# Kernel optimization log

Hardware: AMD Instinct MI355X
Metric: run time of the kernel (lower is better)

The kernel has to match this reference:

```python
import jax, jax.numpy as jnp
import numpy as np
import math

EPS = 1e-5  # BatchNorm eps; eval mode with running_mean=0, running_var=1


def maxpool(x, k, p):
    return jax.lax.reduce_window(x, -jnp.inf, jax.lax.max,
                                 (1, 1, k, k), (1, 1, 1, 1),
                                 ((0, 0), (0, 0), (p, p), (p, p)))


def conv1x1(x, w, b=None):
    # x: [B,Cin,H,W], w: [Cout,Cin]
    y = jnp.einsum('oi,bihw->bohw', w, x)
    if b is not None:
        y = y + b[None, :, None, None]
    return y


def bn_eval(x, g, b):
    scale = g / jnp.sqrt(1.0 + EPS)
    return x * scale[None, :, None, None] + b[None, :, None, None]


def setup_inputs() -> dict:
    B, C, H, W = 2, 64, 80, 80
    c1, c2, c3 = 21, 21, 22
    ch = 32  # C//2
    ks = jax.random.split(jax.random.key(0), 16)
    s = 0.05
    inp = {
        'x': jax.random.normal(ks[0], (B, C, H, W), jnp.float32),
        'q1_w': jax.random.normal(ks[1], (c1, c1), jnp.float32) * s,
        'q1_g': jnp.ones((c1,), jnp.float32),
        'q1_b': jnp.zeros((c1,), jnp.float32),
        'q2_w': jax.random.normal(ks[2], (c2, c2), jnp.float32) * s,
        'q2_g': jnp.ones((c2,), jnp.float32),
        'q2_b': jnp.zeros((c2,), jnp.float32),
        'q3_w': jax.random.normal(ks[3], (c3, c3), jnp.float32) * s,
        'q3_g': jnp.ones((c3,), jnp.float32),
        'q3_b': jnp.zeros((c3,), jnp.float32),
        'k_hf_w': jax.random.normal(ks[4], (ch, C), jnp.float32) * s,
        'k_hf_b': jnp.zeros((ch,), jnp.float32),
        'k_lf_w': jax.random.normal(ks[5], (C - ch, C), jnp.float32) * s,
        'k_lf_b': jnp.zeros((C - ch,), jnp.float32),
        'k_fuse_w': jax.random.normal(ks[6], (C, C), jnp.float32) * s,
        'k_fuse_b': jnp.zeros((C,), jnp.float32),
        'v_bn_g': jnp.ones((C,), jnp.float32),
        'v_bn_b': jnp.zeros((C,), jnp.float32),
        'v_w': jax.random.normal(ks[7], (C, C), jnp.float32) * s,
        'v_b': jnp.zeros((C,), jnp.float32),
        'out_w': jax.random.normal(ks[8], (C, C), jnp.float32) * s,
        'out_b': jnp.zeros((C,), jnp.float32),
    }
    return inp


def reference(x, q1_w, q1_g, q1_b, q2_w, q2_g, q2_b, q3_w, q3_g, q3_b,
              k_hf_w, k_hf_b, k_lf_w, k_lf_b, k_fuse_w, k_fuse_b,
              v_bn_g, v_bn_b, v_w, v_b, out_w, out_b):
    B, C, H, W = x.shape
    N = H * W
    c1 = q1_w.shape[0]
    c2 = q2_w.shape[0]
    # Q: ThreeGroupConvQ (split -> 1x1 conv (no bias) -> BN -> ReLU -> concat)
    x1, x2, x3 = jnp.split(x, [c1, c1 + c2], axis=1)
    y1 = jax.nn.relu(bn_eval(conv1x1(x1, q1_w), q1_g, q1_b))
    y2 = jax.nn.relu(bn_eval(conv1x1(x2, q2_w), q2_g, q2_b))
    y3 = jax.nn.relu(bn_eval(conv1x1(x3, q3_w), q3_g, q3_b))
    Q = jnp.concatenate([y1, y2, y3], axis=1)
    # K: ThermalStructureExtractor
    p3 = maxpool(x, 3, 1)
    p5 = maxpool(x, 5, 2)
    low = (p3 + p5) * 0.5
    high = conv1x1(x - low, k_hf_w, k_hf_b)
    lowp = conv1x1(low, k_lf_w, k_lf_b)
    K = conv1x1(jnp.concatenate([high, lowp], axis=1), k_fuse_w, k_fuse_b)
    # V: BN -> 1x1 conv
    V = conv1x1(bn_eval(x, v_bn_g, v_bn_b), v_w, v_b)
    # attention over N = H*W spatial tokens, channel features
    Qc = Q.reshape(B, C, N)
    Kc = K.reshape(B, C, N)
    Vc = V.reshape(B, C, N)
    attn = jax.nn.softmax(
        jnp.einsum('bcn,bcm->bnm', Qc, Kc) / math.sqrt(C), axis=-1)  # [B,N,N]
    out = jnp.einsum('bnm,bcm->bcn', attn, Vc).reshape(B, C, H, W)
    return conv1x1(out, out_w, out_b) + x
```

## Files before the change

kernel.cpp:

```cpp
#include <hip/hip_runtime.h>
#include <hip/hip_bf16.h>


#define BATCH 2
#define CH 64
#define HH 80
#define WW 80
#define NN 6400
#define NT 100
#define KS 5
#define KTPS (NT/KS)
#define EPSV 1e-5f
#define NEGBIG (-1e30f)
#define LOG2E8 0.18033688f

typedef __hip_bfloat16 bf16;
typedef __attribute__((ext_vector_type(8))) short short8;
typedef __attribute__((ext_vector_type(4))) float f4;
#define MFMA16 __builtin_amdgcn_mfma_f32_16x16x32_bf16

__device__ __forceinline__ float b2f(bf16 v){ return __bfloat162float(v); }
__device__ __forceinline__ bf16 f2b(float v){ return __float2bfloat16(v); }
__device__ __forceinline__ ushort f2bu(float v){ return ((__hip_bfloat16_raw)__float2bfloat16(v)).x; }
__device__ __forceinline__ float bu2f(ushort u){
  union { unsigned int i; float f; } w; w.i = ((unsigned int)u) << 16; return w.f;
}
__device__ __forceinline__ unsigned pkbf(float a, float b){
  union { __hip_bfloat162 h2; unsigned u; } cv;
  cv.h2 = __float22bfloat162_rn(make_float2(a, b));
  return cv.u;
}
__device__ __forceinline__ float fexp2(float x){
#if __has_builtin(__builtin_amdgcn_exp2f)
  return __builtin_amdgcn_exp2f(x);
#else
  return exp2f(x);
#endif
}
__device__ __forceinline__ int swz(int row, int colb){
  return row*128 + (colb ^ ((row & 7) << 4));
}

#define OFF_BIAS 0
#define OFF_WH_B 768
#define OFF_LOW_B (768 + 32768)
#define OFF_Q_B   (OFF_LOW_B + BATCH*CH*NN*2)
#define OFF_K_B   (OFF_Q_B   + BATCH*CH*NN*2)
#define OFF_V_B   (OFF_K_B   + BATCH*CH*NN*2)
#define OFF_P_B   (OFF_V_B   + BATCH*CH*NN*2)
#define OFF_ML_B  (OFF_P_B   + BATCH*NT*KS*4096*2)

__global__ __launch_bounds__(256) void setup_fold(
    const float* __restrict__ q1w, const float* __restrict__ q1g, const float* __restrict__ q1b,
    const float* __restrict__ q2w, const float* __restrict__ q2g, const float* __restrict__ q2b,
    const float* __restrict__ q3w, const float* __restrict__ q3g, const float* __restrict__ q3b,
    const float* __restrict__ khw, const float* __restrict__ khb,
    const float* __restrict__ klw, const float* __restrict__ klb,
    const float* __restrict__ kfw, const float* __restrict__ kfb,
    const float* __restrict__ vg,  const float* __restrict__ vbnb,
    const float* __restrict__ vw,  const float* __restrict__ vb,
    const float* __restrict__ outw,
    float* __restrict__ biasf, bf16* __restrict__ wh)
{
  __shared__ __align__(16) float skf[4096];
  __shared__ __align__(16) float skh[2048];
  __shared__ __align__(16) float skl[2048];
  __shared__ __align__(16) float sow[4096];
  __shared__ __align__(16) float svw[4096];
  __shared__ float sbv[64];

  int tid = threadIdx.x;
  int blk = blockIdx.x;
  #pragma unroll
  for (int i = 0; i < 4; ++i) {
    *(float4*)&skf[(i*256 + tid)*4] = *(const float4*)&kfw[(i*256 + tid)*4];
    *(float4*)&sow[(i*256 + tid)*4] = *(const float4*)&outw[(i*256 + tid)*4];
    *(float4*)&svw[(i*256 + tid)*4] = *(const float4*)&vw[(i*256 + tid)*4];
  }
  #pragma unroll
  for (int i = 0; i < 2; ++i) {
    *(float4*)&skh[(i*256 + tid)*4] = *(const float4*)&khw[(i*256 + tid)*4];
    *(float4*)&skl[(i*256 + tid)*4] = *(const float4*)&klw[(i*256 + tid)*4];
  }
  __syncthreads();

  float rs = rsqrtf(1.0f + EPSV);
  if (tid < 64) {
    int j = tid;
    float bvo = vb[j];
    for (int ci2 = 0; ci2 < 64; ++ci2) bvo += svw[j*64 + ci2] * vbnb[ci2];
    sbv[j] = bvo;
  }

  bf16* wq   = wh;
  bf16* wvp  = wh + 4096;
  bf16* wa1  = wh + 8192;
  bf16* wa2m = wh + 12288;

  int t = blk*256 + tid;
  int ci = t & 63, co = t >> 6;
  int o = co*64 + ci;

  float w = 0.f, g;
  if (co < 21)      { g = q1g[co];    w = (ci < 21)              ? q1w[co*21 + ci]            : 0.f; }
  else if (co < 42) { g = q2g[co-21]; w = (ci >= 21 && ci < 42)  ? q2w[(co-21)*21 + (ci-21)]  : 0.f; }
  else              { g = q3g[co-42]; w = (ci >= 42)             ? q3w[(co-42)*22 + (ci-42)]  : 0.f; }
  wq[o] = f2b(w * g * rs * LOG2E8);

  float a1 = 0.f, a2 = 0.f;
  #pragma unroll
  for (int j = 0; j < 32; ++j) {
    a1 += skf[co*64 + j]      * skh[j*64 + ci];
    a2 += skf[co*64 + 32 + j] * skl[j*64 + ci];
  }
  wa1[o]  = f2b(a1);
  wa2m[o] = f2b(a2 - a1);

  float av = 0.f;
  #pragma unroll
  for (int j = 0; j < 64; ++j)
    av += sow[co*64 + j] * svw[j*64 + ci];
  wvp[o] = f2b(av * vg[ci] * rs);

  if (blk == 0 && tid < 64) {
    int c2 = tid;
    float bq;
    if (c2 < 21)      bq = q1b[c2];
    else if (c2 < 42) bq = q2b[c2-21];
    else              bq = q3b[c2-42];
    biasf[c2] = bq * LOG2E8;
    float bk = kfb[c2];
    #pragma unroll
    for (int j = 0; j < 32; ++j) {
      bk += skf[c2*64 + j]      * khb[j];
      bk += skf[c2*64 + 32 + j] * klb[j];
    }
    biasf[64 + c2] = bk;
    float bvp = 0.f;
    #pragma unroll
    for (int j = 0; j < 64; ++j) bvp += sow[c2*64 + j] * sbv[j];
    biasf[128 + c2] = bvp;
  }
}

__global__ __launch_bounds__(256) void pool_low(const float* __restrict__ x,
                                                bf16* __restrict__ lowg)
{
  int t4 = (blockIdx.x*256 + threadIdx.x)*4;
  int bc = t4 / NN; int n = t4 % NN;
  int h = n / WW, w0 = n % WW;
  const float* p = x + bc*NN;
  float m5[4], m3[4];
  #pragma unroll
  for (int j=0;j<4;++j){ m5[j]=NEGBIG; m3[j]=NEGBIG; }
  #pragma unroll
  for (int dh = -2; dh <= 2; ++dh) {
    int hh = h + dh; if (hh < 0 || hh >= HH) continue;
    float r[12];
    const float* row = p + hh*WW;
    if (w0 >= 4)      { float4 a = *(const float4*)&row[w0-4]; r[0]=a.x;r[1]=a.y;r[2]=a.z;r[3]=a.w; }
    else              { r[0]=NEGBIG;r[1]=NEGBIG;r[2]=NEGBIG;r[3]=NEGBIG; }
    { float4 a = *(const float4*)&row[w0]; r[4]=a.x;r[5]=a.y;r[6]=a.z;r[7]=a.w; }
    if (w0 + 7 < WW)  { float4 a = *(const float4*)&row[w0+4]; r[8]=a.x;r[9]=a.y;r[10]=a.z;r[11]=a.w; }
    else              { r[8]=NEGBIG;r[9]=NEGBIG;r[10]=NEGBIG;r[11]=NEGBIG; }
    bool in3 = (dh >= -1 && dh <= 1);
    #pragma unroll
    for (int j=0;j<4;++j) {
      float v3 = fmaxf(fmaxf(r[3+j], r[4+j]), r[5+j]);
      float v5 = fmaxf(fmaxf(r[2+j], v3), r[6+j]);
      m5[j] = fmaxf(m5[j], v5);
      if (in3) m3[j] = fmaxf(m3[j], v3);
    }
  }
  ushort4 o;
  o.x = f2bu(0.5f*(m3[0]+m5[0]));
  o.y = f2bu(0.5f*(m3[1]+m5[1]));
  o.z = f2bu(0.5f*(m3[2]+m5[2]));
  o.w = f2bu(0.5f*(m3[3]+m5[3]));
  *(ushort4*)&lowg[t4] = o;
}

__global__ __launch_bounds__(256, 2) void qkv_kernel(
    const float* __restrict__ x, const float* __restrict__ biasf,
    const bf16* __restrict__ wh, const bf16* __restrict__ lowg,
    bf16* __restrict__ qgT, bf16* __restrict__ kgT, bf16* __restrict__ vgc)
{
  __shared__ __align__(16) char xT[8192];
  __shared__ __align__(16) char lT[8192];
  __shared__ float bias[192];

  int tid = threadIdx.x;
  int blk = blockIdx.x;
  int b = blk / NT, tile = blk % NT;
  int n0 = tile*64;
  int wv = tid >> 6, lane = tid & 63, ln = lane & 15, quad = lane >> 4;

  if (tid < 192) bias[tid] = biasf[tid];

  {
    int cq = tid & 15, nq = tid >> 4;
    const float* xp = x + (size_t)(b*CH + cq*4)*NN + n0 + nq*4;
    float4 x0 = *(const float4*)&xp[0*NN];
    float4 x1 = *(const float4*)&xp[(size_t)1*NN];
    float4 x2 = *(const float4*)&xp[(size_t)2*NN];
    float4 x3 = *(const float4*)&xp[(size_t)3*NN];
    const bf16* lp = lowg + (size_t)(b*CH + cq*4)*NN + n0 + nq*4;
    uint2 l0 = *(const uint2*)&lp[0*NN];
    uint2 l1 = *(const uint2*)&lp[(size_t)1*NN];
    uint2 l2 = *(const uint2*)&lp[(size_t)2*NN];
    uint2 l3 = *(const uint2*)&lp[(size_t)3*NN];
    uint2 w;
    w.x = pkbf(x0.x, x1.x); w.y = pkbf(x2.x, x3.x);
    *(uint2*)(xT + swz(nq*4+0, cq*8)) = w;
    w.x = (l0.x & 0xffffu) | ((l1.x & 0xffffu) << 16);
    w.y = (l2.x & 0xffffu) | ((l3.x & 0xffffu) << 16);
    *(uint2*)(lT + swz(nq*4+0, cq*8)) = w;
    w.x = pkbf(x0.y, x1.y); w.y = pkbf(x2.y, x3.y);
    *(uint2*)(xT + swz(nq*4+1, cq*8)) = w;
    w.x = (l0.x >> 16) | ((l1.x >> 16) << 16);
    w.y = (l2.x >> 16) | ((l3.x >> 16) << 16);
    *(uint2*)(lT + swz(nq*4+1, cq*8)) = w;
    w.x = pkbf(x0.z, x1.z); w.y = pkbf(x2.z, x3.z);
    *(uint2*)(xT + swz(nq*4+2, cq*8)) = w;
    w.x = (l0.y & 0xffffu) | ((l1.y & 0xffffu) << 16);
    w.y = (l2.y & 0xffffu) | ((l3.y & 0xffffu) << 16);
    *(uint2*)(lT + swz(nq*4+2, cq*8)) = w;
    w.x = pkbf(x0.w, x1.w); w.y = pkbf(x2.w, x3.w);
    *(uint2*)(xT + swz(nq*4+3, cq*8)) = w;
    w.x = (l0.y >> 16) | ((l1.y >> 16) << 16);
    w.y = (l2.y >> 16) | ((l3.y >> 16) << 16);
    *(uint2*)(lT + swz(nq*4+3, cq*8)) = w;
  }
  __syncthreads();

  short8 xb00 = *(const short8*)(xT + swz(0*16 + ln, quad*16));
  short8 xb01 = *(const short8*)(xT + swz(0*16 + ln, 64 + quad*16));
  short8 xb10 = *(const short8*)(xT + swz(1*16 + ln, quad*16));
  short8 xb11 = *(const short8*)(xT + swz(1*16 + ln, 64 + quad*16));
  short8 xb20 = *(const short8*)(xT + swz(2*16 + ln, quad*16));
  short8 xb21 = *(const short8*)(xT + swz(2*16 + ln, 64 + quad*16));
  short8 xb30 = *(const short8*)(xT + swz(3*16 + ln, quad*16));
  short8 xb31 = *(const short8*)(xT + swz(3*16 + ln, 64 + quad*16));
  short8 xa0 = *(const short8*)(xT + swz(wv*16 + ln, quad*16));
  short8 xa1 = *(const short8*)(xT + swz(wv*16 + ln, 64 + quad*16));

  int cb = wv*16 + quad*4;
  const bf16* wqp  = wh;
  const bf16* wvpp = wh + 4096;
  const bf16* wa1p = wh + 8192;
  const bf16* wa2p = wh + 12288;
  int wrow = (wv*16 + ln)*64;

  {
    {
      short8 w0 = *(const short8*)&wvpp[(0*16 + ln)*64 + quad*8];
      short8 w1 = *(const short8*)&wvpp[(0*16 + ln)*64 + 32 + quad*8];
      float bv = bias[128 + 0*16 + ln];
      f4 a = (f4){bv, bv, bv, bv};
      a = MFMA16(xa0, w0, a, 0, 0, 0);
      a = MFMA16(xa1, w1, a, 0, 0, 0);
      uint2 pk; pk.x = pkbf(a[0], a[1]); pk.y = pkbf(a[2], a[3]);
      *(uint2*)&vgc[(size_t)(b*CH + 0*16 + ln)*NN + n0 + cb] = pk;
    }
    {
      short8 w0 = *(const short8*)&wvpp[(1*16 + ln)*64 + quad*8];
      short8 w1 = *(const short8*)&wvpp[(1*16 + ln)*64 + 32 + quad*8];
      float bv = bias[128 + 1*16 + ln];
      f4 a = (f4){bv, bv, bv, bv};
      a = MFMA16(xa0, w0, a, 0, 0, 0);
      a = MFMA16(xa1, w1, a, 0, 0, 0);
      uint2 pk; pk.x = pkbf(a[0], a[1]); pk.y = pkbf(a[2], a[3]);
      *(uint2*)&vgc[(size_t)(b*CH + 1*16 + ln)*NN + n0 + cb] = pk;
    }
    {
      short8 w0 = *(const short8*)&wvpp[(2*16 + ln)*64 + quad*8];
      short8 w1 = *(const short8*)&wvpp[(2*16 + ln)*64 + 32 + quad*8];
      float bv = bias[128 + 2*16 + ln];
      f4 a = (f4){bv, bv, bv, bv};
      a = MFMA16(xa0, w0, a, 0, 0, 0);
      a = MFMA16(xa1, w1, a, 0, 0, 0);
      uint2 pk; pk.x = pkbf(a[0], a[1]); pk.y = pkbf(a[2], a[3]);
      *(uint2*)&vgc[(size_t)(b*CH + 2*16 + ln)*NN + n0 + cb] = pk;
    }
    {
      short8 w0 = *(const short8*)&wvpp[(3*16 + ln)*64 + quad*8];
      short8 w1 = *(const short8*)&wvpp[(3*16 + ln)*64 + 32 + quad*8];
      float bv = bias[128 + 3*16 + ln];
      f4 a = (f4){bv, bv, bv, bv};
      a = MFMA16(xa0, w0, a, 0, 0, 0);
      a = MFMA16(xa1, w1, a, 0, 0, 0);
      uint2 pk; pk.x = pkbf(a[0], a[1]); pk.y = pkbf(a[2], a[3]);
      *(uint2*)&vgc[(size_t)(b*CH + 3*16 + ln)*NN + n0 + cb] = pk;
    }
  }

  {
    short8 wq0 = *(const short8*)&wqp[wrow + quad*8];
    short8 wq1 = *(const short8*)&wqp[wrow + 32 + quad*8];
    f4 bQ;
    bQ[0] = bias[cb+0]; bQ[1] = bias[cb+1]; bQ[2] = bias[cb+2]; bQ[3] = bias[cb+3];
    {
      f4 a = bQ;
      a = MFMA16(wq0, xb00, a, 0, 0, 0);
      a = MFMA16(wq1, xb01, a, 0, 0, 0);
      uint2 pk;
      pk.x = pkbf(fmaxf(a[0],0.f), fmaxf(a[1],0.f));
      pk.y = pkbf(fmaxf(a[2],0.f), fmaxf(a[3],0.f));
      *(uint2*)&qgT[(size_t)(b*NN + n0 + 0*16 + ln)*64 + cb] = pk;
    }
    {
      f4 a = bQ;
      a = MFMA16(wq0, xb10, a, 0, 0, 0);
      a = MFMA16(wq1, xb11, a, 0, 0, 0);
      uint2 pk;
      pk.x = pkbf(fmaxf(a[0],0.f), fmaxf(a[1],0.f));
      pk.y = pkbf(fmaxf(a[2],0.f), fmaxf(a[3],0.f));
      *(uint2*)&qgT[(size_t)(b*NN + n0 + 1*16 + ln)*64 + cb] = pk;
    }
    {
      f4 a = bQ;
      a = MFMA16(wq0, xb20, a, 0, 0, 0);
      a = MFMA16(wq1, xb21, a, 0, 0, 0);
      uint2 pk;
      pk.x = pkbf(fmaxf(a[0],0.f), fmaxf(a[1],0.f));
      pk.y = pkbf(fmaxf(a[2],0.f), fmaxf(a[3],0.f));
      *(uint2*)&qgT[(size_t)(b*NN + n0 + 2*16 + ln)*64 + cb] = pk;
    }
    {
      f4 a = bQ;
      a = MFMA16(wq0, xb30, a, 0, 0, 0);
      a = MFMA16(wq1, xb31, a, 0, 0, 0);
      uint2 pk;
      pk.x = pkbf(fmaxf(a[0],0.f), fmaxf(a[1],0.f));
      pk.y = pkbf(fmaxf(a[2],0.f), fmaxf(a[3],0.f));
      *(uint2*)&qgT[(size_t)(b*NN + n0 + 3*16 + ln)*64 + cb] = pk;
    }
  }

  {
    short8 wa10 = *(const short8*)&wa1p[wrow + quad*8];
    short8 wa11 = *(const short8*)&wa1p[wrow + 32 + quad*8];
    short8 wm0  = *(const short8*)&wa2p[wrow + quad*8];
    short8 wm1  = *(const short8*)&wa2p[wrow + 32 + quad*8];
    short8 lb00 = *(const short8*)(lT + swz(0*16 + ln, quad*16));
    short8 lb01 = *(const short8*)(lT + swz(0*16 + ln, 64 + quad*16));
    short8 lb10 = *(const short8*)(lT + swz(1*16 + ln, quad*16));
    short8 lb11 = *(const short8*)(lT + swz(1*16 + ln, 64 + quad*16));
    short8 lb20 = *(const short8*)(lT + swz(2*16 + ln, quad*16));
    short8 lb21 = *(const short8*)(lT + swz(2*16 + ln, 64 + quad*16));
    short8 lb30 = *(const short8*)(lT + swz(3*16 + ln, quad*16));
    short8 lb31 = *(const short8*)(lT + swz(3*16 + ln, 64 + quad*16));
    f4 bK;
    bK[0] = bias[64+cb+0]; bK[1] = bias[64+cb+1];
    bK[2] = bias[64+cb+2]; bK[3] = bias[64+cb+3];
    {
      f4 a = bK;
      a = MFMA16(wa10, xb00, a, 0, 0, 0);
      a = MFMA16(wa11, xb01, a, 0, 0, 0);
      a = MFMA16(wm0,  lb00, a, 0, 0, 0);
      a = MFMA16(wm1,  lb01, a, 0, 0, 0);
      uint2 pk; pk.x = pkbf(a[0], a[1]); pk.y = pkbf(a[2], a[3]);
      *(uint2*)&kgT[(size_t)(b*NN + n0 + 0*16 + ln)*64 + cb] = pk;
    }
    {
      f4 a = bK;
      a = MFMA16(wa10, xb10, a, 0, 0, 0);
      a = MFMA16(wa11, xb11, a, 0, 0, 0);
      a = MFMA16(wm0,  lb10, a, 0, 0, 0);
      a = MFMA16(wm1,  lb11, a, 0, 0, 0);
      uint2 pk; pk.x = pkbf(a[0], a[1]); pk.y = pkbf(a[2], a[3]);
      *(uint2*)&kgT[(size_t)(b*NN + n0 + 1*16 + ln)*64 + cb] = pk;
    }
    {
      f4 a = bK;
      a = MFMA16(wa10, xb20, a, 0, 0, 0);
      a = MFMA16(wa11, xb21, a, 0, 0, 0);
      a = MFMA16(wm0,  lb20, a, 0, 0, 0);
      a = MFMA16(wm1,  lb21, a, 0, 0, 0);
      uint2 pk; pk.x = pkbf(a[0], a[1]); pk.y = pkbf(a[2], a[3]);
      *(uint2*)&kgT[(size_t)(b*NN + n0 + 2*16 + ln)*64 + cb] = pk;
    }
    {
      f4 a = bK;
      a = MFMA16(wa10, xb30, a, 0, 0, 0);
      a = MFMA16(wa11, xb31, a, 0, 0, 0);
      a = MFMA16(wm0,  lb30, a, 0, 0, 0);
      a = MFMA16(wm1,  lb31, a, 0, 0, 0);
      uint2 pk; pk.x = pkbf(a[0], a[1]); pk.y = pkbf(a[2], a[3]);
      *(uint2*)&kgT[(size_t)(b*NN + n0 + 3*16 + ln)*64 + cb] = pk;
    }
  }
}

__global__ __launch_bounds__(256, 2) void attn_partial(
    const bf16* __restrict__ qgT, const bf16* __restrict__ kgT, const bf16* __restrict__ vgc,
    ushort* __restrict__ part, float* __restrict__ pml)
{
  __shared__ __align__(16) char smem[32768];
  __shared__ float lred[256];

  int tid = threadIdx.x;
  int blk = blockIdx.x;
  int b = blk / (NT*KS);
  int rem = blk % (NT*KS);
  int tile = rem / KS, split = rem % KS;
  int n0 = tile*64;
  int wv = tid >> 6, lane = tid & 63, ln = lane & 15, quad = lane >> 4;
  int mbase = split*KTPS*64;

  int r0 = tid >> 3,         c0 = (tid & 7)*8;
  int r1 = 32 + (tid >> 3),  c1 = (tid & 7)*8;

  {
    uint4 qa = *(const uint4*)&qgT[(size_t)(b*NN + n0 + r0)*64 + c0];
    uint4 qb = *(const uint4*)&qgT[(size_t)(b*NN + n0 + r1)*64 + c1];
    *(uint4*)(smem + swz(r0, c0*2)) = qa;
    *(uint4*)(smem + swz(r1, c1*2)) = qb;
  }
  __syncthreads();
  short8 bq00 = *(const short8*)(smem + swz( 0*16 + ln, quad*16));
  short8 bq01 = *(const short8*)(smem + swz( 0*16 + ln, 64 + quad*16));
  short8 bq10 = *(const short8*)(smem + swz( 1*16 + ln, quad*16));
  short8 bq11 = *(const short8*)(smem + swz( 1*16 + ln, 64 + quad*16));
  short8 bq20 = *(const short8*)(smem + swz( 2*16 + ln, quad*16));
  short8 bq21 = *(const short8*)(smem + swz( 2*16 + ln, 64 + quad*16));
  short8 bq30 = *(const short8*)(smem + swz( 3*16 + ln, quad*16));
  short8 bq31 = *(const short8*)(smem + swz( 3*16 + ln, 64 + quad*16));
  {
    uint4 va  = *(const uint4*)&vgc[(size_t)(b*CH + r0)*NN + mbase + c0];
    uint4 vb4 = *(const uint4*)&vgc[(size_t)(b*CH + r1)*NN + mbase + c1];
    *(uint4*)(smem + 16384 + swz(r0, c0*2)) = va;
    *(uint4*)(smem + 16384 + swz(r1, c1*2)) = vb4;
  }
  const bf16* kb = kgT + (size_t)(b*NN + mbase + wv*16 + ln)*64;
  short8 ak0 = *(const short8*)&kb[quad*8];
  short8 ak1 = *(const short8*)&kb[32 + quad*8];
  __syncthreads();

  f4 accO0 = (f4){0.f,0.f,0.f,0.f};
  f4 accO1 = (f4){0.f,0.f,0.f,0.f};
  f4 accO2 = (f4){0.f,0.f,0.f,0.f};
  f4 accO3 = (f4){0.f,0.f,0.f,0.f};
  float lacc0 = 0.f, lacc1 = 0.f, lacc2 = 0.f, lacc3 = 0.f;

  uint4 vr0, vr1;
  short8 an0, an1;
  for (int kt = 0; kt < KTPS; ++kt) {
    const int po = (kt & 1) * 8192;
    const int vo = 16384 + (kt & 1) * 8192;
    {
      int ktn = (kt + 1 < KTPS) ? kt + 1 : kt;
      int m1 = mbase + ktn*64;
      vr0 = *(const uint4*)&vgc[(size_t)(b*CH + r0)*NN + m1 + c0];
      vr1 = *(const uint4*)&vgc[(size_t)(b*CH + r1)*NN + m1 + c1];
      an0 = *(const short8*)&kb[(size_t)ktn*4096 + quad*8];
      an1 = *(const short8*)&kb[(size_t)ktn*4096 + 32 + quad*8];
    }

    f4 accS0, accS1, accS2, accS3;
    {
      f4 z = (f4){0.f,0.f,0.f,0.f};
      z = MFMA16(ak0, bq00, z, 0, 0, 0);
      accS0 = MFMA16(ak1, bq01, z, 0, 0, 0);
    }
    {
      f4 z = (f4){0.f,0.f,0.f,0.f};
      z = MFMA16(ak0, bq10, z, 0, 0, 0);
      accS1 = MFMA16(ak1, bq11, z, 0, 0, 0);
    }
    {
      f4 z = (f4){0.f,0.f,0.f,0.f};
      z = MFMA16(ak0, bq20, z, 0, 0, 0);
      accS2 = MFMA16(ak1, bq21, z, 0, 0, 0);
    }
    {
      f4 z = (f4){0.f,0.f,0.f,0.f};
      z = MFMA16(ak0, bq30, z, 0, 0, 0);
      accS3 = MFMA16(ak1, bq31, z, 0, 0, 0);
    }
    {
      float p0 = fexp2(accS0[0]), p1 = fexp2(accS0[1]);
      float p2 = fexp2(accS0[2]), p3 = fexp2(accS0[3]);
      lacc0 += (p0 + p1) + (p2 + p3);
      uint2 pk; pk.x = pkbf(p0, p1); pk.y = pkbf(p2, p3);
      *(uint2*)(smem + po + swz(0*16 + ln, wv*32 + quad*8)) = pk;
    }
    {
      float p0 = fexp2(accS1[0]), p1 = fexp2(accS1[1]);
      float p2 = fexp2(accS1[2]), p3 = fexp2(accS1[3]);
      lacc1 += (p0 + p1) + (p2 + p3);
      uint2 pk; pk.x = pkbf(p0, p1); pk.y = pkbf(p2, p3);
      *(uint2*)(smem + po + swz(1*16 + ln, wv*32 + quad*8)) = pk;
    }
    {
      float p0 = fexp2(accS2[0]), p1 = fexp2(accS2[1]);
      float p2 = fexp2(accS2[2]), p3 = fexp2(accS2[3]);
      lacc2 += (p0 + p1) + (p2 + p3);
      uint2 pk; pk.x = pkbf(p0, p1); pk.y = pkbf(p2, p3);
      *(uint2*)(smem + po + swz(2*16 + ln, wv*32 + quad*8)) = pk;
    }
    {
      float p0 = fexp2(accS3[0]), p1 = fexp2(accS3[1]);
      float p2 = fexp2(accS3[2]), p3 = fexp2(accS3[3]);
      lacc3 += (p0 + p1) + (p2 + p3);
      uint2 pk; pk.x = pkbf(p0, p1); pk.y = pkbf(p2, p3);
      *(uint2*)(smem + po + swz(3*16 + ln, wv*32 + quad*8)) = pk;
    }
    __syncthreads();

    short8 ap0 = *(const short8*)(smem + po + swz(wv*16 + ln, quad*16));
    short8 ap1 = *(const short8*)(smem + po + swz(wv*16 + ln, 64 + quad*16));
    {
      short8 bv0 = *(const short8*)(smem + vo + swz(0*16 + ln, quad*16));
      short8 bv1 = *(const short8*)(smem + vo + swz(0*16 + ln, 64 + quad*16));
      accO0 = MFMA16(ap0, bv0, accO0, 0, 0, 0);
      accO0 = MFMA16(ap1, bv1, accO0, 0, 0, 0);
    }
    {
      short8 bv0 = *(const short8*)(smem + vo + swz(1*16 + ln, quad*16));
      short8 bv1 = *(const short8*)(smem + vo + swz(1*16 + ln, 64 + quad*16));
      accO1 = MFMA16(ap0, bv0, accO1, 0, 0, 0);
      accO1 = MFMA16(ap1, bv1, accO1, 0, 0, 0);
    }
    {
      short8 bv0 = *(const short8*)(smem + vo + swz(2*16 + ln, quad*16));
      short8 bv1 = *(const short8*)(smem + vo + swz(2*16 + ln, 64 + quad*16));
      accO2 = MFMA16(ap0, bv0, accO2, 0, 0, 0);
      accO2 = MFMA16(ap1, bv1, accO2, 0, 0, 0);
    }
    {
      short8 bv0 = *(const short8*)(smem + vo + swz(3*16 + ln, quad*16));
      short8 bv1 = *(const short8*)(smem + vo + swz(3*16 + ln, 64 + quad*16));
      accO3 = MFMA16(ap0, bv0, accO3, 0, 0, 0);
      accO3 = MFMA16(ap1, bv1, accO3, 0, 0, 0);
    }
    if (kt + 1 < KTPS) {
      int vn = 16384 + ((kt+1) & 1) * 8192;
      *(uint4*)(smem + vn + swz(r0, c0*2)) = vr0;
      *(uint4*)(smem + vn + swz(r1, c1*2)) = vr1;
    }
    ak0 = an0; ak1 = an1;
  }

  size_t pbase = ((size_t)(b*NT + tile)*KS + split)*4096;
  ushort* pp = part + pbase;
  {
    uint2 pk; pk.x = pkbf(accO0[0], accO0[1]); pk.y = pkbf(accO0[2], accO0[3]);
    *(uint2*)&pp[(0*16 + ln)*64 + wv*16 + quad*4] = pk;
  }
  {
    uint2 pk; pk.x = pkbf(accO1[0], accO1[1]); pk.y = pkbf(accO1[2], accO1[3]);
    *(uint2*)&pp[(1*16 + ln)*64 + wv*16 + quad*4] = pk;
  }
  {
    uint2 pk; pk.x = pkbf(accO2[0], accO2[1]); pk.y = pkbf(accO2[2], accO2[3]);
    *(uint2*)&pp[(2*16 + ln)*64 + wv*16 + quad*4] = pk;
  }
  {
    uint2 pk; pk.x = pkbf(accO3[0], accO3[1]); pk.y = pkbf(accO3[2], accO3[3]);
    *(uint2*)&pp[(3*16 + ln)*64 + wv*16 + quad*4] = pk;
  }
  {
    float s = lacc0;
    s += __shfl_xor(s, 16); s += __shfl_xor(s, 32);
    if (quad == 0) lred[wv*64 + 0*16 + ln] = s;
  }
  {
    float s = lacc1;
    s += __shfl_xor(s, 16); s += __shfl_xor(s, 32);
    if (quad == 0) lred[wv*64 + 1*16 + ln] = s;
  }
  {
    float s = lacc2;
    s += __shfl_xor(s, 16); s += __shfl_xor(s, 32);
    if (quad == 0) lred[wv*64 + 2*16 + ln] = s;
  }
  {
    float s = lacc3;
    s += __shfl_xor(s, 16); s += __shfl_xor(s, 32);
    if (quad == 0) lred[wv*64 + 3*16 + ln] = s;
  }
  __syncthreads();
  if (tid < 64) {
    size_t mlb = ((size_t)(b*NT + tile)*KS + split)*64;
    pml[mlb + tid] = (lred[tid] + lred[64 + tid]) + (lred[128 + tid] + lred[192 + tid]);
  }
}

__global__ __launch_bounds__(256) void attn_reduce(
    const ushort* __restrict__ part, const float* __restrict__ pml,
    const float* __restrict__ x, const float* __restrict__ outb,
    float* __restrict__ out)
{
  __shared__ float linv[64];
  __shared__ float ob[64];

  int tid = threadIdx.x;
  int blk = blockIdx.x;
  int b = blk / NT, tile = blk % NT;
  size_t base = (size_t)(b*NT + tile)*KS;

  if (tid < 64) {
    float l = 0.f;
    #pragma unroll
    for (int s=0;s<KS;++s) l += pml[(base+s)*64 + tid];
    linv[tid] = 1.0f / l;
    ob[tid] = outb[tid];
  }
  __syncthreads();

  #pragma unroll
  for (int j = 0; j < 4; ++j) {
    int idx = j*256 + tid;
    int c = idx >> 4, q = idx & 15;
    float a0=0.f, a1=0.f, a2=0.f, a3=0.f;
    #pragma unroll
    for (int s = 0; s < KS; ++s) {
      uint2 v = *(const uint2*)&part[(base+s)*4096 + (size_t)c*64 + q*4];
      a0 += bu2f((ushort)(v.x & 0xffff)); a1 += bu2f((ushort)(v.x >> 16));
      a2 += bu2f((ushort)(v.y & 0xffff)); a3 += bu2f((ushort)(v.y >> 16));
    }
    int nl = q*4;
    size_t gidx = (size_t)(b*CH + c)*NN + tile*64 + nl;
    float4 xv = *(const float4*)&x[gidx];
    float bc = ob[c];
    float4 o;
    o.x = a0*linv[nl+0] + bc + xv.x;
    o.y = a1*linv[nl+1] + bc + xv.y;
    o.z = a2*linv[nl+2] + bc + xv.z;
    o.w = a3*linv[nl+3] + bc + xv.w;
    *(float4*)&out[gidx] = o;
  }
}

extern "C" void kernel_launch(void* const* d_in, const int* in_sizes, int n_in,
                              void* d_out, int out_size, void* d_ws, size_t ws_size,
                              hipStream_t stream) {
  const float* x    = (const float*)d_in[0];
  const float* q1w  = (const float*)d_in[1];
  const float* q1g  = (const float*)d_in[2];
  const float* q1b  = (const float*)d_in[3];
  const float* q2w  = (const float*)d_in[4];
  const float* q2g  = (const float*)d_in[5];
  const float* q2b  = (const float*)d_in[6];
  const float* q3w  = (const float*)d_in[7];
  const float* q3g  = (const float*)d_in[8];
  const float* q3b  = (const float*)d_in[9];
  const float* khw  = (const float*)d_in[10];
  const float* khb  = (const float*)d_in[11];
  const float* klw  = (const float*)d_in[12];
  const float* klb  = (const float*)d_in[13];
  const float* kfw  = (const float*)d_in[14];
  const float* kfb  = (const float*)d_in[15];
  const float* vbg  = (const float*)d_in[16];
  const float* vbb  = (const float*)d_in[17];
  const float* vw   = (const float*)d_in[18];
  const float* vb   = (const float*)d_in[19];
  const float* outw = (const float*)d_in[20];
  const float* outb = (const float*)d_in[21];

  char*   wsb  = (char*)d_ws;
  float*  biasf= (float*)(wsb + OFF_BIAS);
  bf16*   wh   = (bf16*)(wsb + OFF_WH_B);
  bf16*   lowg = (bf16*)(wsb + OFF_LOW_B);
  bf16*   qgT  = (bf16*)(wsb + OFF_Q_B);
  bf16*   kgT  = (bf16*)(wsb + OFF_K_B);
  bf16*   vgc  = (bf16*)(wsb + OFF_V_B);
  ushort* part = (ushort*)(wsb + OFF_P_B);
  float*  pml  = (float*)(wsb + OFF_ML_B);

  hipLaunchKernelGGL(setup_fold, dim3(16), dim3(256), 0, stream,
                     q1w,q1g,q1b,q2w,q2g,q2b,q3w,q3g,q3b,
                     khw,khb,klw,klb,kfw,kfb,vbg,vbb,vw,vb,outw, biasf, wh);
  hipLaunchKernelGGL(pool_low, dim3(BATCH*CH*NN/1024), dim3(256), 0, stream, x, lowg);
  hipLaunchKernelGGL(qkv_kernel, dim3(BATCH*NT), dim3(256), 0, stream,
                     x, biasf, wh, lowg, qgT, kgT, vgc);
  hipLaunchKernelGGL(attn_partial, dim3(BATCH*NT*KS), dim3(256), 0, stream,
                     qgT, kgT, vgc, part, pml);
  hipLaunchKernelGGL(attn_reduce, dim3(BATCH*NT), dim3(256), 0, stream,
                     part, pml, x, outb, (float*)d_out);
}
```

Before: 147.9 us.

## Store V in tiled MFMA-ready layout and load operands directly from global

After: 209.6 us. +41.7%, slower.

```diff
diff --git a/kernel.cpp b/kernel.cpp
--- a/kernel.cpp
+++ b/kernel.cpp
@@ -250,6 +250,7 @@
   const bf16* wa1p = wh + 8192;
   const bf16* wa2p = wh + 12288;
   int wrow = (wv*16 + ln)*64;
+  size_t vtile = (size_t)(b*NT + tile)*4096;
 
   {
     {
@@ -260,7 +261,7 @@
       a = MFMA16(xa0, w0, a, 0, 0, 0);
       a = MFMA16(xa1, w1, a, 0, 0, 0);
       uint2 pk; pk.x = pkbf(a[0], a[1]); pk.y = pkbf(a[2], a[3]);
-      *(uint2*)&vgc[(size_t)(b*CH + 0*16 + ln)*NN + n0 + cb] = pk;
+      *(uint2*)&vgc[vtile + (0*16 + ln)*64 + cb] = pk;
     }
     {
       short8 w0 = *(const short8*)&wvpp[(1*16 + ln)*64 + quad*8];
@@ -270,7 +271,7 @@
       a = MFMA16(xa0, w0, a, 0, 0, 0);
       a = MFMA16(xa1, w1, a, 0, 0, 0);
       uint2 pk; pk.x = pkbf(a[0], a[1]); pk.y = pkbf(a[2], a[3]);
-      *(uint2*)&vgc[(size_t)(b*CH + 1*16 + ln)*NN + n0 + cb] = pk;
+      *(uint2*)&vgc[vtile + (1*16 + ln)*64 + cb] = pk;
     }
     {
       short8 w0 = *(const short8*)&wvpp[(2*16 + ln)*64 + quad*8];
@@ -280,7 +281,7 @@
       a = MFMA16(xa0, w0, a, 0, 0, 0);
       a = MFMA16(xa1, w1, a, 0, 0, 0);
       uint2 pk; pk.x = pkbf(a[0], a[1]); pk.y = pkbf(a[2], a[3]);
-      *(uint2*)&vgc[(size_t)(b*CH + 2*16 + ln)*NN + n0 + cb] = pk;
+      *(uint2*)&vgc[vtile + (2*16 + ln)*64 + cb] = pk;
     }
     {
       short8 w0 = *(const short8*)&wvpp[(3*16 + ln)*64 + quad*8];
@@ -290,7 +291,7 @@
       a = MFMA16(xa0, w0, a, 0, 0, 0);
       a = MFMA16(xa1, w1, a, 0, 0, 0);
       uint2 pk; pk.x = pkbf(a[0], a[1]); pk.y = pkbf(a[2], a[3]);
-      *(uint2*)&vgc[(size_t)(b*CH + 3*16 + ln)*NN + n0 + cb] = pk;
+      *(uint2*)&vgc[vtile + (3*16 + ln)*64 + cb] = pk;
     }
   }
 
@@ -396,7 +397,7 @@
     const bf16* __restrict__ qgT, const bf16* __restrict__ kgT, const bf16* __restrict__ vgc,
     ushort* __restrict__ part, float* __restrict__ pml)
 {
-  __shared__ __align__(16) char smem[32768];
+  __shared__ __align__(16) char smem[16384];
   __shared__ float lred[256];
 
   int tid = threadIdx.x;
@@ -426,15 +427,10 @@
   short8 bq21 = *(const short8*)(smem + swz( 2*16 + ln, 64 + quad*16));
   short8 bq30 = *(const short8*)(smem + swz( 3*16 + ln, quad*16));
   short8 bq31 = *(const short8*)(smem + swz( 3*16 + ln, 64 + quad*16));
-  {
-    uint4 va  = *(const uint4*)&vgc[(size_t)(b*CH + r0)*NN + mbase + c0];
-    uint4 vb4 = *(const uint4*)&vgc[(size_t)(b*CH + r1)*NN + mbase + c1];
-    *(uint4*)(smem + 16384 + swz(r0, c0*2)) = va;
-    *(uint4*)(smem + 16384 + swz(r1, c1*2)) = vb4;
-  }
   const bf16* kb = kgT + (size_t)(b*NN + mbase + wv*16 + ln)*64;
   short8 ak0 = *(const short8*)&kb[quad*8];
   short8 ak1 = *(const short8*)&kb[32 + quad*8];
+  const bf16* vt = vgc + (size_t)(b*NT + split*KTPS)*4096 + ln*64 + quad*8;
   __syncthreads();
 
   f4 accO0 = (f4){0.f,0.f,0.f,0.f};
@@ -443,16 +439,20 @@
   f4 accO3 = (f4){0.f,0.f,0.f,0.f};
   float lacc0 = 0.f, lacc1 = 0.f, lacc2 = 0.f, lacc3 = 0.f;
 
-  uint4 vr0, vr1;
   short8 an0, an1;
   for (int kt = 0; kt < KTPS; ++kt) {
     const int po = (kt & 1) * 8192;
-    const int vo = 16384 + (kt & 1) * 8192;
+    const bf16* vk = vt + (size_t)kt*4096;
+    short8 bv00 = *(const short8*)&vk[0*1024];
+    short8 bv01 = *(const short8*)&vk[0*1024 + 32];
+    short8 bv10 = *(const short8*)&vk[1*1024];
+    short8 bv11 = *(const short8*)&vk[1*1024 + 32];
+    short8 bv20 = *(const short8*)&vk[2*1024];
+    short8 bv21 = *(const short8*)&vk[2*1024 + 32];
+    short8 bv30 = *(const short8*)&vk[3*1024];
+    short8 bv31 = *(const short8*)&vk[3*1024 + 32];
     {
       int ktn = (kt + 1 < KTPS) ? kt + 1 : kt;
-      int m1 = mbase + ktn*64;
-      vr0 = *(const uint4*)&vgc[(size_t)(b*CH + r0)*NN + m1 + c0];
-      vr1 = *(const uint4*)&vgc[(size_t)(b*CH + r1)*NN + m1 + c1];
       an0 = *(const short8*)&kb[(size_t)ktn*4096 + quad*8];
       an1 = *(const short8*)&kb[(size_t)ktn*4096 + 32 + quad*8];
     }
@@ -510,35 +510,14 @@
 
     short8 ap0 = *(const short8*)(smem + po + swz(wv*16 + ln, quad*16));
     short8 ap1 = *(const short8*)(smem + po + swz(wv*16 + ln, 64 + quad*16));
-    {
-      short8 bv0 = *(const short8*)(smem + vo + swz(0*16 + ln, quad*16));
-      short8 bv1 = *(const short8*)(smem + vo + swz(0*16 + ln, 64 + quad*16));
-      accO0 = MFMA16(ap0, bv0, accO0, 0, 0, 0);
-      accO0 = MFMA16(ap1, bv1, accO0, 0, 0, 0);
-    }
-    {
-      short8 bv0 = *(const short8*)(smem + vo + swz(1*16 + ln, quad*16));
-      short8 bv1 = *(const short8*)(smem + vo + swz(1*16 + ln, 64 + quad*16));
-      accO1 = MFMA16(ap0, bv0, accO1, 0, 0, 0);
-      accO1 = MFMA16(ap1, bv1, accO1, 0, 0, 0);
-    }
-    {
-      short8 bv0 = *(const short8*)(smem + vo + swz(2*16 + ln, quad*16));
-      short8 bv1 = *(const short8*)(smem + vo + swz(2*16 + ln, 64 + quad*16));
-      accO2 = MFMA16(ap0, bv0, accO2, 0, 0, 0);
-      accO2 = MFMA16(ap1, bv1, accO2, 0, 0, 0);
-    }
-    {
-      short8 bv0 = *(const short8*)(smem + vo + swz(3*16 + ln, quad*16));
-      short8 bv1 = *(const short8*)(smem + vo + swz(3*16 + ln, 64 + quad*16));
-      accO3 = MFMA16(ap0, bv0, accO3, 0, 0, 0);
-      accO3 = MFMA16(ap1, bv1, accO3, 0, 0, 0);
-    }
-    if (kt + 1 < KTPS) {
-      int vn = 16384 + ((kt+1) & 1) * 8192;
-      *(uint4*)(smem + vn + swz(r0, c0*2)) = vr0;
-      *(uint4*)(smem + vn + swz(r1, c1*2)) = vr1;
-    }
+    accO0 = MFMA16(ap0, bv00, accO0, 0, 0, 0);
+    accO0 = MFMA16(ap1, bv01, accO0, 0, 0, 0);
+    accO1 = MFMA16(ap0, bv10, accO1, 0, 0, 0);
+    accO1 = MFMA16(ap1, bv11, accO1, 0, 0, 0);
+    accO2 = MFMA16(ap0, bv20, accO2, 0, 0, 0);
+    accO2 = MFMA16(ap1, bv21, accO2, 0, 0, 0);
+    accO3 = MFMA16(ap0, bv30, accO3, 0, 0, 0);
+    accO3 = MFMA16(ap1, bv31, accO3, 0, 0, 0);
     ak0 = an0; ak1 = an1;
   }
 
```
